# Kernel optimization log

Hardware: AMD Instinct MI355X
Metric: run time of the kernel (lower is better)

The kernel has to match this reference:

```python
import jax, jax.numpy as jnp
import numpy as np

EPS = 1e-6

def setup_inputs() -> dict:
    key = jax.random.key(0)
    k1, k2 = jax.random.split(key)
    patch_feats = jax.random.normal(k1, (576, 768), dtype=jnp.float32)   # [N, D] ViT-B/16 @ 384 -> 24x24 patches
    memory = jax.random.normal(k2, (200000, 768), dtype=jnp.float32)     # [M, D] coreset memory bank
    return {"patch_feats": patch_feats, "memory": memory, "topk": 10}

def reference(patch_feats, memory, topk):
    # L2-normalize both sides (same eps placement as torch: x / (||x|| + eps))
    f = patch_feats / (jnp.linalg.norm(patch_feats, axis=1, keepdims=True) + EPS)  # [N, D]
    m = memory / (jnp.linalg.norm(memory, axis=1, keepdims=True) + EPS)            # [M, D]
    # cosine distance = 1 - sim; min over memory bank. Equivalent to the chunked
    # min-of-mins in the original (min is associative over chunks).
    sim = jnp.einsum('nd,md->nm', f, m)          # [N, M]
    patch_scores = jnp.min(1.0 - sim, axis=1)    # [N]
    # image score: mean of top-k patch scores
    k = min(topk, patch_scores.shape[0])
    topk_vals = jax.lax.top_k(patch_scores, k)[0]
    image_score = jnp.mean(topk_vals)
    return (patch_scores, image_score)
```

## Files before the change

### kernel.cpp

```cpp
#include <hip/hip_runtime.h>
#include <hip/hip_bf16.h>

#define DD 768
#define NPATCH 576
#define BMR 64
#define NSLAB 24
#define EPSF 1e-6f
#define NRB 384

typedef short bf16x8 __attribute__((ext_vector_type(8)));
typedef float f32x4 __attribute__((ext_vector_type(4)));

__device__ __forceinline__ unsigned short f2bf(float x) {
  __hip_bfloat16 h = __float2bfloat16(x);
  return __builtin_bit_cast(unsigned short, h);
}

__global__ __launch_bounds__(256) void k_norm(const float* __restrict__ pf,
                                              float* __restrict__ invn) {
  int row = blockIdx.x;
  int t = threadIdx.x;
  const float* src = pf + (size_t)row * DD;
  float v0 = src[t], v1 = src[t + 256], v2 = src[t + 512];
  float ss = v0 * v0 + v1 * v1 + v2 * v2;
#pragma unroll
  for (int m = 1; m < 64; m <<= 1) ss += __shfl_xor(ss, m, 64);
  __shared__ float wss[4];
  if ((t & 63) == 0) wss[t >> 6] = ss;
  __syncthreads();
  if (t == 0) {
    float tot = wss[0] + wss[1] + wss[2] + wss[3];
    invn[row] = 1.0f / (sqrtf(tot) + EPSF);
  }
}

__global__ __launch_bounds__(256) void k_pack(const float* __restrict__ pf,
                                              const float* __restrict__ invn,
                                              unsigned short* __restrict__ Fws) {
  int bid = blockIdx.x;
  int ks = bid / 36, ptg = bid % 36;
  int t = threadIdx.x;
  int i = t * 2;
  int s = i >> 3, j = i & 7;
  int p = ptg * 16 + (s & 15);
  int k = ks * 32 + (s >> 4) * 8 + j;
  float sc = invn[p];
  float a0 = pf[(size_t)p * DD + k] * sc;
  float a1 = pf[(size_t)p * DD + k + 1] * sc;
  unsigned int outw = (unsigned int)f2bf(a0) | ((unsigned int)f2bf(a1) << 16);
  ((unsigned int*)Fws)[(size_t)bid * 256 + t] = outw;
}

#define PACK_BW(bw, u0, u1)                                               \
  bw.x = (unsigned int)f2bf(u0.x) | ((unsigned int)f2bf(u0.y) << 16);     \
  bw.y = (unsigned int)f2bf(u0.z) | ((unsigned int)f2bf(u0.w) << 16);     \
  bw.z = (unsigned int)f2bf(u1.x) | ((unsigned int)f2bf(u1.y) << 16);     \
  bw.w = (unsigned int)f2bf(u1.z) | ((unsigned int)f2bf(u1.w) << 16);

#define SQ8(u0, u1)                                                        \
  (u0.x * u0.x + u0.y * u0.y + u0.z * u0.z + u0.w * u0.w +                 \
   u1.x * u1.x + u1.y * u1.y + u1.z * u1.z + u1.w * u1.w)

#define KSTEP(ks, buf, I0, I1, C0, C1)                                     \
  {                                                                        \
    const unsigned short* Ak = Abase + (size_t)(ks) * (36 * 512);          \
    bf16x8 ar[9];                                                          \
    _Pragma("unroll")                                                      \
    for (int p = 0; p < 9; ++p) ar[p] = *(const bf16x8*)(Ak + p * 512);    \
    __builtin_amdgcn_sched_barrier(0);     \
    if ((ks) + 2 < NSLAB) {                                                \
      const float* g = gsrc + ((ks) + 2) * 32;                             \
      I0 = *(const float4*)g;                                              \
      I1 = *(const float4*)(g + 4);                                        \
    }                                                                      \
    bf16x8 b0 = *(const bf16x8*)((const char*)Bs[buf] + rbyte0);           \
    bf16x8 b1 = *(const bf16x8*)((const char*)Bs[buf] + rbyte1);           \
    _Pragma("unroll")                                                      \
    for (int p = 0; p < 9; ++p) {                                          \
      acc[p][0] = __builtin_amdgcn_mfma_f32_16x16x32_bf16(ar[p], b0, acc[p][0], 0, 0, 0); \
      acc[p][1] = __builtin_amdgcn_mfma_f32_16x16x32_bf16(ar[p], b1, acc[p][1], 0, 0, 0); \
    }                                                                      \
    if ((ks) < NSLAB - 1) {                                                \
      ssr += SQ8(C0, C1);                                                  \
      uint4 bw;                                                            \
      PACK_BW(bw, C0, C1);                                                 \
      *(uint4*)((char*)Bs[(buf) ^ 1] + wbyte) = bw;                        \
    }                                                                      \
    __syncthreads();                                                       \
  }

__global__ __launch_bounds__(256, 3) void k_main(const unsigned short* __restrict__ Fws,
                                                 const float* __restrict__ mem,
                                                 float* __restrict__ partial,
                                                 int M, int nchunk) {
  __shared__ __align__(16) unsigned short Bs[2][2048];
  __shared__ float smin[2][288];
  __shared__ float ssq[BMR];

  int t = threadIdx.x;
  int l = t & 63, l15 = l & 15, lhi = l >> 4;
  int w = t >> 6, pw = w & 1, rw = w >> 1;
  int c = blockIdx.x & 1, rb = blockIdx.x >> 1;
  int srow = t >> 2, sq = t & 3;

  for (int i = t; i < 2 * 288; i += 256) ((float*)smin)[i] = 1e30f;

  const unsigned short* Abase =
      Fws + (size_t)(c * 18 + pw * 9) * 512 + (size_t)(lhi * 16 + l15) * 8;

  int rbyte0, rbyte1;
  {
    int sw = ((l15 & 7) << 4);
    rbyte0 = (rw * 2 + 0) * 1024 + ((l15 * 64 + lhi * 16) ^ sw);
    rbyte1 = (rw * 2 + 1) * 1024 + ((l15 * 64 + lhi * 16) ^ sw);
  }
  int wl15 = srow & 15;
  int wbyte = (srow >> 4) * 1024 + ((wl15 * 64 + sq * 16) ^ ((wl15 & 7) << 4));

#pragma unroll 1
  for (int chunk = rb; chunk < nchunk; chunk += NRB) {
    int grow = chunk * BMR + srow;
    if (grow > M - 1) grow = M - 1;
    const float* gsrc = mem + (size_t)grow * DD + sq * 8;
    float ssr = 0.f;

    float4 P0, P1, Q0, Q1;
    P0 = *(const float4*)(gsrc);
    P1 = *(const float4*)(gsrc + 4);
    Q0 = *(const float4*)(gsrc + 32);
    Q1 = *(const float4*)(gsrc + 36);
    ssr += SQ8(P0, P1);
    {
      uint4 bw;
      PACK_BW(bw, P0, P1);
      *(uint4*)((char*)Bs[0] + wbyte) = bw;
    }
    __syncthreads();

    f32x4 acc[9][2];
#pragma unroll
    for (int p = 0; p < 9; ++p) {
      f32x4 z = {0.f, 0.f, 0.f, 0.f};
      acc[p][0] = z;
      acc[p][1] = z;
    }

#pragma unroll 1
    for (int ks = 0; ks < NSLAB; ks += 2) {
      KSTEP(ks, 0, P0, P1, Q0, Q1);
      KSTEP(ks + 1, 1, Q0, Q1, P0, P1);
    }

    float s2 = ssr + __shfl_xor(ssr, 1, 64);
    s2 += __shfl_xor(s2, 2, 64);
    if (sq == 0) ssq[srow] = s2;
    __syncthreads();

    float inv0, inv1;
    bool ok0, ok1;
    {
      int rl0 = (rw * 2 + 0) * 16 + l15;
      int rl1 = (rw * 2 + 1) * 16 + l15;
      inv0 = 1.0f / (sqrtf(ssq[rl0]) + EPSF);
      inv1 = 1.0f / (sqrtf(ssq[rl1]) + EPSF);
      ok0 = (chunk * BMR + rl0) < M;
      ok1 = (chunk * BMR + rl1) < M;
    }
#pragma unroll
    for (int p = 0; p < 9; ++p) {
#pragma unroll
      for (int q = 0; q < 4; ++q) {
        float e0 = ok0 ? (1.0f - acc[p][0][q] * inv0) : 1e30f;
        float e1 = ok1 ? (1.0f - acc[p][1][q] * inv1) : 1e30f;
        float d = fminf(e0, e1);
        d = fminf(d, __shfl_xor(d, 1, 64));
        d = fminf(d, __shfl_xor(d, 2, 64));
        d = fminf(d, __shfl_xor(d, 4, 64));
        d = fminf(d, __shfl_xor(d, 8, 64));
        if (l15 == 0) {
          int pl = (pw * 9 + p) * 16 + lhi * 4 + q;
          smin[rw][pl] = fminf(smin[rw][pl], d);
        }
      }
    }
    __syncthreads();
  }

  for (int i = t; i < 288; i += 256)
    partial[(size_t)rb * NPATCH + c * 288 + i] = fminf(smin[0][i], smin[1][i]);
}

__global__ __launch_bounds__(256) void k_colmin(const float* __restrict__ partial,
                                                float* __restrict__ out, int nb) {
  int p = blockIdx.x;
  int t = threadIdx.x;
  float v = 1e30f;
  for (int b = t; b < nb; b += 256) v = fminf(v, partial[(size_t)b * NPATCH + p]);
#pragma unroll
  for (int m = 1; m < 64; m <<= 1) v = fminf(v, __shfl_xor(v, m, 64));
  __shared__ float wmin[4];
  if ((t & 63) == 0) wmin[t >> 6] = v;
  __syncthreads();
  if (t == 0) out[p] = fminf(fminf(wmin[0], wmin[1]), fminf(wmin[2], wmin[3]));
}

__global__ __launch_bounds__(256) void k_topk(float* __restrict__ out,
                                              const int* __restrict__ topk_p) {
  __shared__ float vals[NPATCH];
  __shared__ float wv[4];
  __shared__ int wi[4];
  __shared__ float ssum;
  int t = threadIdx.x;
  for (int p = t; p < NPATCH; p += 256) vals[p] = out[p];
  if (t == 0) ssum = 0.f;
  int k = topk_p[0];
  if (k > NPATCH) k = NPATCH;
  if (k < 1) k = 1;
  __syncthreads();
  for (int it = 0; it < k; ++it) {
    float bv = -1e30f;
    int bi = 0;
    for (int p = t; p < NPATCH; p += 256) {
      float x = vals[p];
      if (x > bv) { bv = x; bi = p; }
    }
#pragma unroll
    for (int m = 1; m < 64; m <<= 1) {
      float ov = __shfl_xor(bv, m, 64);
      int oi = __shfl_xor(bi, m, 64);
      if (ov > bv || (ov == bv && oi < bi)) { bv = ov; bi = oi; }
    }
    if ((t & 63) == 0) { wv[t >> 6] = bv; wi[t >> 6] = bi; }
    __syncthreads();
    if (t == 0) {
      float fbv = wv[0]; int fbi = wi[0];
      for (int q = 1; q < 4; ++q)
        if (wv[q] > fbv || (wv[q] == fbv && wi[q] < fbi)) { fbv = wv[q]; fbi = wi[q]; }
      ssum += fbv;
      vals[fbi] = -1e30f;
    }
    __syncthreads();
  }
  if (t == 0) out[NPATCH] = ssum / (float)k;
}

extern "C" void kernel_launch(void* const* d_in, const int* in_sizes, int n_in,
                              void* d_out, int out_size, void* d_ws, size_t ws_size,
                              hipStream_t stream) {
  const float* pf = (const float*)d_in[0];
  const float* mem = (const float*)d_in[1];
  const int* topk = (const int*)d_in[2];
  float* out = (float*)d_out;
  int M = in_sizes[1] / DD;
  int nchunk = (M + BMR - 1) / BMR;

  unsigned short* Fws = (unsigned short*)d_ws;
  float* invn = (float*)((char*)d_ws + 884736);
  float* partial = (float*)((char*)d_ws + 884736 + 2304);

  k_norm<<<NPATCH, 256, 0, stream>>>(pf, invn);
  k_pack<<<864, 256, 0, stream>>>(pf, invn, Fws);
  k_main<<<2 * NRB, 256, 0, stream>>>(Fws, mem, partial, M, nchunk);
  k_colmin<<<NPATCH, 256, 0, stream>>>(partial, out, NRB);
  k_topk<<<1, 256, 0, stream>>>(out, topk);
}
```

Before: 370.5 us.

## Double-buffer A fragments and deepen memory-bank prefetch to three stages

Restructures the main k-loop so the A (patch) fragments for the next slab are loaded into a second register set while the current slab's MFMAs run, and the memory-bank global prefetch goes three slabs ahead instead of two, with a rotating P/Q/R register triple. Syncthreads is replaced by explicit lgkmcnt waits, sched barriers and s_barrier to pin the issue order. The extra registers lower the occupancy target from 3 to 2 blocks per SM and the grid shrinks from 384 to 256 row-blocks per half. This trades occupancy for latency hiding inside each wave.

```diff
diff --git a/kernel.cpp b/kernel.cpp
--- a/kernel.cpp
+++ b/kernel.cpp
@@ -6,7 +6,7 @@
 #define BMR 64
 #define NSLAB 24
 #define EPSF 1e-6f
-#define NRB 384
+#define NRB 256
 
 typedef short bf16x8 __attribute__((ext_vector_type(8)));
 typedef float f32x4 __attribute__((ext_vector_type(4)));
@@ -61,35 +61,41 @@
   (u0.x * u0.x + u0.y * u0.y + u0.z * u0.z + u0.w * u0.w +                 \
    u1.x * u1.x + u1.y * u1.y + u1.z * u1.z + u1.w * u1.w)
 
-#define KSTEP(ks, buf, I0, I1, C0, C1)                                     \
+#define KSTEP(n, buf, ARC, ARN, C0, C1, I0, I1)                            \
   {                                                                        \
-    const unsigned short* Ak = Abase + (size_t)(ks) * (36 * 512);          \
-    bf16x8 ar[9];                                                          \
-    _Pragma("unroll")                                                      \
-    for (int p = 0; p < 9; ++p) ar[p] = *(const bf16x8*)(Ak + p * 512);    \
-    __builtin_amdgcn_sched_barrier(0);     \
-    if ((ks) + 2 < NSLAB) {                                                \
-      const float* g = gsrc + ((ks) + 2) * 32;                             \
+    if ((n) + 1 < NSLAB) {                                                 \
+      const unsigned short* An = Abase + (size_t)((n) + 1) * (36 * 512);   \
+      _Pragma("unroll")                                                    \
+      for (int p = 0; p < 9; ++p) ARN[p] = *(const bf16x8*)(An + p * 512); \
+    }                                                                      \
+    __builtin_amdgcn_sched_barrier(0);                                     \
+    if ((n) + 3 < NSLAB) {                                                 \
+      const float* g = gsrc + ((n) + 3) * 32;                              \
       I0 = *(const float4*)g;                                              \
       I1 = *(const float4*)(g + 4);                                        \
     }                                                                      \
-    bf16x8 b0 = *(const bf16x8*)((const char*)Bs[buf] + rbyte0);           \
-    bf16x8 b1 = *(const bf16x8*)((const char*)Bs[buf] + rbyte1);           \
-    _Pragma("unroll")                                                      \
-    for (int p = 0; p < 9; ++p) {                                          \
-      acc[p][0] = __builtin_amdgcn_mfma_f32_16x16x32_bf16(ar[p], b0, acc[p][0], 0, 0, 0); \
-      acc[p][1] = __builtin_amdgcn_mfma_f32_16x16x32_bf16(ar[p], b1, acc[p][1], 0, 0, 0); \
-    }                                                                      \
-    if ((ks) < NSLAB - 1) {                                                \
+    __builtin_amdgcn_sched_barrier(0);                                     \
+    if ((n) < NSLAB - 1) {                                                 \
       ssr += SQ8(C0, C1);                                                  \
       uint4 bw;                                                            \
       PACK_BW(bw, C0, C1);                                                 \
       *(uint4*)((char*)Bs[(buf) ^ 1] + wbyte) = bw;                        \
     }                                                                      \
-    __syncthreads();                                                       \
-  }
-
-__global__ __launch_bounds__(256, 3) void k_main(const unsigned short* __restrict__ Fws,
+    __builtin_amdgcn_sched_barrier(0);                                     \
+    bf16x8 b0 = *(const bf16x8*)((const char*)Bs[buf] + rbyte0);           \
+    bf16x8 b1 = *(const bf16x8*)((const char*)Bs[buf] + rbyte1);           \
+    asm volatile("s_waitcnt lgkmcnt(0)" ::: "memory");                     \
+    __builtin_amdgcn_sched_barrier(0);                                     \
+    _Pragma("unroll")                                                      \
+    for (int p = 0; p < 9; ++p) {                                          \
+      acc[p][0] = __builtin_amdgcn_mfma_f32_16x16x32_bf16(ARC[p], b0, acc[p][0], 0, 0, 0); \
+      acc[p][1] = __builtin_amdgcn_mfma_f32_16x16x32_bf16(ARC[p], b1, acc[p][1], 0, 0, 0); \
+    }                                                                      \
+    __builtin_amdgcn_sched_barrier(0);                                     \
+    __builtin_amdgcn_s_barrier();                                          \
+  }
+
+__global__ __launch_bounds__(256, 2) void k_main(const unsigned short* __restrict__ Fws,
                                                  const float* __restrict__ mem,
                                                  float* __restrict__ partial,
                                                  int M, int nchunk) {
@@ -124,18 +130,32 @@
     const float* gsrc = mem + (size_t)grow * DD + sq * 8;
     float ssr = 0.f;
 
-    float4 P0, P1, Q0, Q1;
+    float4 P0, P1, Q0, Q1, R0, R1;
+    bf16x8 arA[9], arB[9];
+
     P0 = *(const float4*)(gsrc);
     P1 = *(const float4*)(gsrc + 4);
+    __builtin_amdgcn_sched_barrier(0);
+    {
+      const unsigned short* A0 = Abase;
+#pragma unroll
+      for (int p = 0; p < 9; ++p) arA[p] = *(const bf16x8*)(A0 + p * 512);
+    }
+    __builtin_amdgcn_sched_barrier(0);
     Q0 = *(const float4*)(gsrc + 32);
     Q1 = *(const float4*)(gsrc + 36);
+    R0 = *(const float4*)(gsrc + 64);
+    R1 = *(const float4*)(gsrc + 68);
+    __builtin_amdgcn_sched_barrier(0);
     ssr += SQ8(P0, P1);
     {
       uint4 bw;
       PACK_BW(bw, P0, P1);
       *(uint4*)((char*)Bs[0] + wbyte) = bw;
     }
-    __syncthreads();
+    asm volatile("s_waitcnt lgkmcnt(0)" ::: "memory");
+    __builtin_amdgcn_sched_barrier(0);
+    __builtin_amdgcn_s_barrier();
 
     f32x4 acc[9][2];
 #pragma unroll
@@ -146,10 +166,20 @@
     }
 
 #pragma unroll 1
-    for (int ks = 0; ks < NSLAB; ks += 2) {
-      KSTEP(ks, 0, P0, P1, Q0, Q1);
-      KSTEP(ks + 1, 1, Q0, Q1, P0, P1);
-    }
+    for (int n = 0; n < 18; n += 6) {
+      KSTEP(n + 0, 0, arA, arB, Q0, Q1, P0, P1);
+      KSTEP(n + 1, 1, arB, arA, R0, R1, Q0, Q1);
+      KSTEP(n + 2, 0, arA, arB, P0, P1, R0, R1);
+      KSTEP(n + 3, 1, arB, arA, Q0, Q1, P0, P1);
+      KSTEP(n + 4, 0, arA, arB, R0, R1, Q0, Q1);
+      KSTEP(n + 5, 1, arB, arA, P0, P1, R0, R1);
+    }
+    KSTEP(18, 0, arA, arB, Q0, Q1, P0, P1);
+    KSTEP(19, 1, arB, arA, R0, R1, Q0, Q1);
+    KSTEP(20, 0, arA, arB, P0, P1, R0, R1);
+    KSTEP(21, 1, arB, arA, Q0, Q1, P0, P1);
+    KSTEP(22, 0, arA, arB, R0, R1, Q0, Q1);
+    KSTEP(23, 1, arB, arA, P0, P1, R0, R1);
 
     float s2 = ssr + __shfl_xor(ssr, 1, 64);
     s2 += __shfl_xor(s2, 2, 64);
```

After: 586.5 us. 1.58x slower.

## Deepen global prefetch to three slabs and reorder LDS store before MFMA

Applied to the files above, without the earlier changes.

Global loads of memory-bank slabs are now issued three k-steps ahead using four rotating register pairs instead of two, so global latency has more MFMA work to hide behind. Within each step, the bf16 pack and LDS store for the next slab now happen before the MFMAs, fenced with sched_barriers. An explicit lgkmcnt wait plus a raw s_barrier replaces __syncthreads. The cost is more live VGPRs, which may pressure occupancy at launch bounds of 3 waves, and a rigid schedule imposed by the sched_barrier fences.

```diff
diff --git a/kernel.cpp b/kernel.cpp
--- a/kernel.cpp
+++ b/kernel.cpp
@@ -61,32 +61,37 @@
   (u0.x * u0.x + u0.y * u0.y + u0.z * u0.z + u0.w * u0.w +                 \
    u1.x * u1.x + u1.y * u1.y + u1.z * u1.z + u1.w * u1.w)
 
-#define KSTEP(ks, buf, I0, I1, C0, C1)                                     \
+#define KSTEP(n, buf, C0, C1, I0, I1)                                      \
   {                                                                        \
-    const unsigned short* Ak = Abase + (size_t)(ks) * (36 * 512);          \
+    const unsigned short* Ak = Abase + (size_t)(n) * (36 * 512);           \
     bf16x8 ar[9];                                                          \
     _Pragma("unroll")                                                      \
     for (int p = 0; p < 9; ++p) ar[p] = *(const bf16x8*)(Ak + p * 512);    \
     __builtin_amdgcn_sched_barrier(0);     \
-    if ((ks) + 2 < NSLAB) {                                                \
-      const float* g = gsrc + ((ks) + 2) * 32;                             \
+    if ((n) + 3 < NSLAB) {                                                 \
+      const float* g = gsrc + ((n) + 3) * 32;                              \
       I0 = *(const float4*)g;                                              \
       I1 = *(const float4*)(g + 4);                                        \
     }                                                                      \
+    __builtin_amdgcn_sched_barrier(0);                                     \
+    if ((n) < NSLAB - 1) {                                                 \
+      ssr += SQ8(C0, C1);                                                  \
+      uint4 bw;                                                            \
+      PACK_BW(bw, C0, C1);                                                 \
+      *(uint4*)((char*)Bs[(buf) ^ 1] + wbyte) = bw;                        \
+    }                                                                      \
+    __builtin_amdgcn_sched_barrier(0);                                     \
     bf16x8 b0 = *(const bf16x8*)((const char*)Bs[buf] + rbyte0);           \
     bf16x8 b1 = *(const bf16x8*)((const char*)Bs[buf] + rbyte1);           \
+    asm volatile("s_waitcnt lgkmcnt(0)" ::: "memory");                     \
+    __builtin_amdgcn_sched_barrier(0);                                     \
     _Pragma("unroll")                                                      \
     for (int p = 0; p < 9; ++p) {                                          \
       acc[p][0] = __builtin_amdgcn_mfma_f32_16x16x32_bf16(ar[p], b0, acc[p][0], 0, 0, 0); \
       acc[p][1] = __builtin_amdgcn_mfma_f32_16x16x32_bf16(ar[p], b1, acc[p][1], 0, 0, 0); \
     }                                                                      \
-    if ((ks) < NSLAB - 1) {                                                \
-      ssr += SQ8(C0, C1);                                                  \
-      uint4 bw;                                                            \
-      PACK_BW(bw, C0, C1);                                                 \
-      *(uint4*)((char*)Bs[(buf) ^ 1] + wbyte) = bw;                        \
-    }                                                                      \
-    __syncthreads();                                                       \
+    __builtin_amdgcn_sched_barrier(0);                                     \
+    __builtin_amdgcn_s_barrier();                                          \
   }
 
 __global__ __launch_bounds__(256, 3) void k_main(const unsigned short* __restrict__ Fws,
@@ -124,18 +129,24 @@
     const float* gsrc = mem + (size_t)grow * DD + sq * 8;
     float ssr = 0.f;
 
-    float4 P0, P1, Q0, Q1;
+    float4 P0, P1, Q0, Q1, R0, R1, T0, T1;
+
     P0 = *(const float4*)(gsrc);
     P1 = *(const float4*)(gsrc + 4);
     Q0 = *(const float4*)(gsrc + 32);
     Q1 = *(const float4*)(gsrc + 36);
+    R0 = *(const float4*)(gsrc + 64);
+    R1 = *(const float4*)(gsrc + 68);
+    __builtin_amdgcn_sched_barrier(0);
     ssr += SQ8(P0, P1);
     {
       uint4 bw;
       PACK_BW(bw, P0, P1);
       *(uint4*)((char*)Bs[0] + wbyte) = bw;
     }
-    __syncthreads();
+    asm volatile("s_waitcnt lgkmcnt(0)" ::: "memory");
+    __builtin_amdgcn_sched_barrier(0);
+    __builtin_amdgcn_s_barrier();
 
     f32x4 acc[9][2];
 #pragma unroll
@@ -146,10 +157,16 @@
     }
 
 #pragma unroll 1
-    for (int ks = 0; ks < NSLAB; ks += 2) {
-      KSTEP(ks, 0, P0, P1, Q0, Q1);
-      KSTEP(ks + 1, 1, Q0, Q1, P0, P1);
-    }
+    for (int n = 0; n < 20; n += 4) {
+      KSTEP(n + 0, 0, Q0, Q1, T0, T1);
+      KSTEP(n + 1, 1, R0, R1, P0, P1);
+      KSTEP(n + 2, 0, T0, T1, Q0, Q1);
+      KSTEP(n + 3, 1, P0, P1, R0, R1);
+    }
+    KSTEP(20, 0, Q0, Q1, T0, T1);
+    KSTEP(21, 1, R0, R1, P0, P1);
+    KSTEP(22, 0, T0, T1, Q0, Q1);
+    KSTEP(23, 1, P0, P1, R0, R1);
 
     float s2 = ssr + __shfl_xor(ssr, 1, 64);
     s2 += __shfl_xor(s2, 2, 64);
```

Result: slower. 506.3 us (+36.6%).
